# Performance work log

Measured on AMD Instinct MI355X. Metric: run time of the kernel, lower is better.

## Reference

```python
import jax, jax.numpy as jnp
import numpy as np

KE = 332.0636  # Coulomb constant in kcal/mol * Angstrom / e^2
N = 4096       # total sites across all frames
F = 64         # number of frames (batch_size)
M = 1024       # number of molecules


def setup_inputs() -> dict:
    key = jax.random.key(0)
    k1, k2, k3, k4, k5 = jax.random.split(key, 5)
    pos = jax.random.normal(k1, (N, 3), dtype=jnp.float32) * 10.0      # Angstrom-scale coords
    charges = jax.random.normal(k2, (N, 1), dtype=jnp.float32) * 0.5    # partial charges
    # lj_params[:, 0] = sigma, lj_params[:, 1] = epsilon (positive)
    lj_params = jax.random.uniform(k3, (N, 2), dtype=jnp.float32, minval=0.1, maxval=1.0)
    frames = jnp.sort(jax.random.randint(k4, (N,), 0, F))               # frame id per site (sorted, as in batching)
    mols = jax.random.randint(k5, (N,), 0, M)                           # molecule id per site
    return {"pos": pos, "charges": charges, "lj_params": lj_params,
            "frames": frames, "mols": mols, "num_frames": F}


def reference(pos, charges, lj_params, frames, mols, num_frames):
    # Dense ordered-pair mask: same frame, different molecule (mirrors torch.nonzero pair set)
    mask = (frames[:, None] == frames[None, :]) & (mols[:, None] != mols[None, :])  # [N, N]
    diff = pos[:, None, :] - pos[None, :, :]                                        # [N, N, 3]
    r2 = jnp.sum(diff * diff, axis=-1)                                              # [N, N]
    r = jnp.sqrt(jnp.where(mask, r2, 1.0))  # masked entries -> safe 1.0 (no div-by-zero / NaN grad)
    # Coulomb: ke * q_i * q_j / r_ij
    q = charges[:, 0]
    coul = KE * (q[:, None] * q[None, :]) / r
    # Lennard-Jones with Lorentz-Berthelot combining: sigma_ij = (s_i+s_j)/2, eps_ij = sqrt(e_i*e_j)
    sig = 0.5 * (lj_params[:, None, 0] + lj_params[None, :, 0])
    eps = jnp.sqrt(lj_params[:, None, 1] * lj_params[None, :, 1])
    sr6 = (sig / r) ** 6
    lj = 4.0 * eps * (sr6 * sr6 - sr6)
    contrib = jnp.where(mask, coul + lj, 0.0)
    # scatter(contribs, frames): pair (i,j) contributes to frame[i]; reduce rows then segment-sum
    per_site = jnp.sum(contrib, axis=1)                                             # [N]
    return jax.ops.segment_sum(per_site, frames, num_segments=num_frames)           # [num_frames]
```

## Files before the change

kernel.cpp:

```cpp
#include <hip/hip_runtime.h>

#define KE_CONST 332.0636f
constexpr int TILE = 256;
constexpr int NT   = 1024;
constexpr int NW   = NT / 64;

__global__ __launch_bounds__(NT) void lj_coul_frame_kernel(
    const float* __restrict__ pos, const float* __restrict__ charges,
    const float* __restrict__ lj, const int* __restrict__ frames,
    const int* __restrict__ mols, float* __restrict__ out, int N)
{
    const int f = blockIdx.x;
    const int tid = threadIdx.x;
    const int lane = tid & 63;
    const int wv = tid >> 6;

    __shared__ float jx[TILE], jy[TILE], jz[TILE], jq[TILE], jsig[TILE], jse[TILE];
    __shared__ int   jmol[TILE];
    __shared__ int   spack[NW];
    __shared__ float wsum[NW];

    int pack = 0;
    {
        const int N4 = N >> 2;
        const int4* f4 = (const int4*)frames;
        for (int k = tid; k < N4; k += NT) {
            const int4 v = f4[k];
            pack += (v.x <  f) + (v.y <  f) + (v.z <  f) + (v.w <  f);
            pack += ((v.x <= f) + (v.y <= f) + (v.z <= f) + (v.w <= f)) << 16;
        }
        for (int k = (N4 << 2) + tid; k < N; k += NT) {
            const int v = frames[k];
            pack += (v < f) + ((v <= f) << 16);
        }
        for (int off = 32; off > 0; off >>= 1)
            pack += __shfl_down(pack, off, 64);
        if (lane == 0) spack[wv] = pack;
        __syncthreads();
    }
    int tot = 0;
    #pragma unroll
    for (int w = 0; w < NW; ++w) tot += spack[w];
    const int lo = tot & 0xFFFF;
    const int hi = tot >> 16;
    const int nf = hi - lo;

    float acc = 0.0f;

    if (nf <= TILE) {
        for (int t = tid; t < nf; t += NT) {
            const int j = lo + t;
            jx[t]   = pos[3 * j + 0];
            jy[t]   = pos[3 * j + 1];
            jz[t]   = pos[3 * j + 2];
            jq[t]   = charges[j];
            jsig[t] = lj[2 * j + 0];
            jse[t]  = sqrtf(lj[2 * j + 1]);
            jmol[t] = mols[j];
        }
        __syncthreads();

        for (int ti = lane; ti < nf; ti += 64) {
            const float xi  = jx[ti];
            const float yi  = jy[ti];
            const float zi  = jz[ti];
            const float ci  = KE_CONST * jq[ti];
            const float si  = jsig[ti];
            const float sei = jse[ti];
            const int   mi  = jmol[ti];

            for (int t = wv; t < nf; t += NW) {
                const float dx = xi - jx[t];
                const float dy = yi - jy[t];
                const float dz = zi - jz[t];
                const float r2 = dx * dx + dy * dy + dz * dz;
                const float inv_r  = rsqrtf(r2);
                const float inv_r2 = inv_r * inv_r;
                const float coul = ci * jq[t] * inv_r;
                const float s    = si + jsig[t];
                const float sr2  = 0.25f * s * s * inv_r2;
                const float sr6  = sr2 * sr2 * sr2;
                const float ljv  = 4.0f * (sei * jse[t]) * (sr6 * sr6 - sr6);
                acc += (mi != jmol[t]) ? (coul + ljv) : 0.0f;
            }
        }
    } else {
        for (int jt = lo; jt < hi; jt += TILE) {
            const int cnt = min(TILE, hi - jt);
            for (int t = tid; t < cnt; t += NT) {
                const int j = jt + t;
                jx[t]   = pos[3 * j + 0];
                jy[t]   = pos[3 * j + 1];
                jz[t]   = pos[3 * j + 2];
                jq[t]   = charges[j];
                jsig[t] = lj[2 * j + 0];
                jse[t]  = sqrtf(lj[2 * j + 1]);
                jmol[t] = mols[j];
            }
            __syncthreads();

            for (int i = lo + lane; i < hi; i += 64) {
                const float xi  = pos[3 * i + 0];
                const float yi  = pos[3 * i + 1];
                const float zi  = pos[3 * i + 2];
                const float ci  = KE_CONST * charges[i];
                const float si  = lj[2 * i + 0];
                const float sei = sqrtf(lj[2 * i + 1]);
                const int   mi  = mols[i];

                for (int t = wv; t < cnt; t += NW) {
                    const float dx = xi - jx[t];
                    const float dy = yi - jy[t];
                    const float dz = zi - jz[t];
                    const float r2 = dx * dx + dy * dy + dz * dz;
                    const float inv_r  = rsqrtf(r2);
                    const float inv_r2 = inv_r * inv_r;
                    const float coul = ci * jq[t] * inv_r;
                    const float s    = si + jsig[t];
                    const float sr2  = 0.25f * s * s * inv_r2;
                    const float sr6  = sr2 * sr2 * sr2;
                    const float ljv  = 4.0f * (sei * jse[t]) * (sr6 * sr6 - sr6);
                    acc += (mi != jmol[t]) ? (coul + ljv) : 0.0f;
                }
            }
            __syncthreads();
        }
    }

    for (int off = 32; off > 0; off >>= 1)
        acc += __shfl_down(acc, off, 64);
    if (lane == 0) wsum[wv] = acc;
    __syncthreads();
    if (tid == 0) {
        float s = 0.0f;
        #pragma unroll
        for (int w = 0; w < NW; ++w) s += wsum[w];
        out[f] = s;
    }
}

extern "C" void kernel_launch(void* const* d_in, const int* in_sizes, int n_in,
                              void* d_out, int out_size, void* d_ws, size_t ws_size,
                              hipStream_t stream) {
    const float* pos     = (const float*)d_in[0];
    const float* charges = (const float*)d_in[1];
    const float* lj      = (const float*)d_in[2];
    const int*   frames  = (const int*)d_in[3];
    const int*   mols    = (const int*)d_in[4];
    const int    N       = in_sizes[3];
    const int    F       = out_size;

    lj_coul_frame_kernel<<<F, NT, 0, stream>>>(pos, charges, lj, frames, mols,
                                               (float*)d_out, N);
}
```

Baseline: 66.35 us.

## Locate frame bounds from a local window instead of scanning all frames

Each block now loads a 512-site window centred on its expected frame position (N/F times the frame index), finds the frame's start and end by comparing neighbouring frame ids, and computes the pair sums from that shared-memory window. This avoids every block reading the whole frames array to count sites before and within its frame. If the frame is not fully inside the window, it falls back to the old full scan with tiled loads. The tile size also grows to 512. The window guess relies on roughly uniform frame sizes; if that fails, the fallback path runs.

Result: no change. 67.02 us (+1.0%).

```diff
diff --git a/kernel.cpp b/kernel.cpp
--- a/kernel.cpp
+++ b/kernel.cpp
@@ -1,9 +1,9 @@
 #include <hip/hip_runtime.h>
 
 #define KE_CONST 332.0636f
-constexpr int TILE = 256;
-constexpr int NT   = 1024;
-constexpr int NW   = NT / 64;
+constexpr int WIN = 512;
+constexpr int NT  = 1024;
+constexpr int NW  = NT / 64;
 
 __global__ __launch_bounds__(NT) void lj_coul_frame_kernel(
     const float* __restrict__ pos, const float* __restrict__ charges,
@@ -15,13 +15,100 @@
     const int lane = tid & 63;
     const int wv = tid >> 6;
 
-    __shared__ float jx[TILE], jy[TILE], jz[TILE], jq[TILE], jsig[TILE], jse[TILE];
-    __shared__ int   jmol[TILE];
+    __shared__ float jx[WIN], jy[WIN], jz[WIN], jq[WIN], jsig[WIN], jse[WIN];
+    __shared__ int   jmol[WIN];
+    __shared__ int   sbound[2];
+    __shared__ int   scov[2];
     __shared__ int   spack[NW];
     __shared__ float wsum[NW];
 
-    int pack = 0;
-    {
+    const int avg    = N / (int)gridDim.x;
+    const int margin = (WIN > avg) ? (WIN - avg) / 2 : 0;
+    int wlo = f * avg - margin;
+    if (wlo < 0) wlo = 0;
+    if (wlo > N - WIN) wlo = (N > WIN) ? (N - WIN) : 0;
+    const int whi  = (wlo + WIN < N) ? (wlo + WIN) : N;
+    const int wcnt = whi - wlo;
+    const bool own = (tid < wcnt);
+
+    int   fk = 0, fk1 = 0x7fffffff, mo = 0;
+    float px = 0.f, py = 0.f, pz = 0.f, qq = 0.f, sg = 0.f, ep = 0.f;
+    if (own) {
+        const int g = wlo + tid;
+        fk  = frames[g];
+        if (g + 1 < N) fk1 = frames[g + 1];
+        px  = pos[3 * g + 0];
+        py  = pos[3 * g + 1];
+        pz  = pos[3 * g + 2];
+        qq  = charges[g];
+        sg  = lj[2 * g + 0];
+        ep  = lj[2 * g + 1];
+        mo  = mols[g];
+    }
+    if (tid < 2) sbound[tid] = -1;
+    __syncthreads();
+
+    if (own) {
+        const int g = wlo + tid;
+        jx[tid]   = px;
+        jy[tid]   = py;
+        jz[tid]   = pz;
+        jq[tid]   = qq;
+        jsig[tid] = sg;
+        jse[tid]  = sqrtf(ep);
+        jmol[tid] = mo;
+
+        if (tid == 0)        scov[0] = (wlo == 0) ? 1 : (fk < f);
+        if (tid == wcnt - 1) scov[1] = (whi == N) ? 1 : (fk > f);
+
+        if (wlo == 0 && tid == 0) {
+            if (fk >= f) sbound[0] = 0;
+            if (fk >  f) sbound[1] = 0;
+        }
+        if (fk <  f && fk1 >= f) sbound[0] = g + 1;
+        if (fk <= f && fk1 >  f) sbound[1] = g + 1;
+    }
+    __syncthreads();
+
+    float acc = 0.0f;
+    const bool covered = (scov[0] != 0) && (scov[1] != 0) &&
+                         (sbound[0] >= 0) && (sbound[1] >= 0);
+
+    if (covered) {
+        const int lo   = sbound[0];
+        const int hi   = sbound[1];
+        int nf   = hi - lo;
+        int base = lo - wlo;
+        if (nf < 0) nf = 0;
+        if (base < 0) base = 0;
+        if (base + nf > wcnt) nf = wcnt - base;
+
+        for (int ti = lane; ti < nf; ti += 64) {
+            const float xi  = jx[base + ti];
+            const float yi  = jy[base + ti];
+            const float zi  = jz[base + ti];
+            const float ci  = KE_CONST * jq[base + ti];
+            const float si  = jsig[base + ti];
+            const float sei = jse[base + ti];
+            const int   mi  = jmol[base + ti];
+
+            for (int t = wv; t < nf; t += NW) {
+                const float dx = xi - jx[base + t];
+                const float dy = yi - jy[base + t];
+                const float dz = zi - jz[base + t];
+                const float r2 = dx * dx + dy * dy + dz * dz;
+                const float inv_r  = rsqrtf(r2);
+                const float inv_r2 = inv_r * inv_r;
+                const float coul = ci * jq[base + t] * inv_r;
+                const float s    = si + jsig[base + t];
+                const float sr2  = 0.25f * s * s * inv_r2;
+                const float sr6  = sr2 * sr2 * sr2;
+                const float ljv  = 4.0f * (sei * jse[base + t]) * (sr6 * sr6 - sr6);
+                acc += (mi != jmol[base + t]) ? (coul + ljv) : 0.0f;
+            }
+        }
+    } else {
+        int pack = 0;
         const int N4 = N >> 2;
         const int4* f4 = (const int4*)frames;
         for (int k = tid; k < N4; k += NT) {
@@ -37,56 +124,15 @@
             pack += __shfl_down(pack, off, 64);
         if (lane == 0) spack[wv] = pack;
         __syncthreads();
-    }
-    int tot = 0;
-    #pragma unroll
-    for (int w = 0; w < NW; ++w) tot += spack[w];
-    const int lo = tot & 0xFFFF;
-    const int hi = tot >> 16;
-    const int nf = hi - lo;
-
-    float acc = 0.0f;
-
-    if (nf <= TILE) {
-        for (int t = tid; t < nf; t += NT) {
-            const int j = lo + t;
-            jx[t]   = pos[3 * j + 0];
-            jy[t]   = pos[3 * j + 1];
-            jz[t]   = pos[3 * j + 2];
-            jq[t]   = charges[j];
-            jsig[t] = lj[2 * j + 0];
-            jse[t]  = sqrtf(lj[2 * j + 1]);
-            jmol[t] = mols[j];
-        }
-        __syncthreads();
-
-        for (int ti = lane; ti < nf; ti += 64) {
-            const float xi  = jx[ti];
-            const float yi  = jy[ti];
-            const float zi  = jz[ti];
-            const float ci  = KE_CONST * jq[ti];
-            const float si  = jsig[ti];
-            const float sei = jse[ti];
-            const int   mi  = jmol[ti];
-
-            for (int t = wv; t < nf; t += NW) {
-                const float dx = xi - jx[t];
-                const float dy = yi - jy[t];
-                const float dz = zi - jz[t];
-                const float r2 = dx * dx + dy * dy + dz * dz;
-                const float inv_r  = rsqrtf(r2);
-                const float inv_r2 = inv_r * inv_r;
-                const float coul = ci * jq[t] * inv_r;
-                const float s    = si + jsig[t];
-                const float sr2  = 0.25f * s * s * inv_r2;
-                const float sr6  = sr2 * sr2 * sr2;
-                const float ljv  = 4.0f * (sei * jse[t]) * (sr6 * sr6 - sr6);
-                acc += (mi != jmol[t]) ? (coul + ljv) : 0.0f;
-            }
-        }
-    } else {
-        for (int jt = lo; jt < hi; jt += TILE) {
-            const int cnt = min(TILE, hi - jt);
+        int tot = 0;
+        #pragma unroll
+        for (int w = 0; w < NW; ++w) tot += spack[w];
+        const int lo = tot & 0xFFFF;
+        const int hi = tot >> 16;
+
+        for (int jt = lo; jt < hi; jt += WIN) {
+            const int cnt = min(WIN, hi - jt);
+            __syncthreads();
             for (int t = tid; t < cnt; t += NT) {
                 const int j = jt + t;
                 jx[t]   = pos[3 * j + 0];
@@ -123,7 +169,6 @@
                     acc += (mi != jmol[t]) ? (coul + ljv) : 0.0f;
                 }
             }
-            __syncthreads();
         }
     }
 
```
